# Kernel optimization log

Measured on AMD Instinct MI355X. Metric: run time of the kernel, lower is better.

Reference implementation:

```python
import jax, jax.numpy as jnp
import numpy as np

N, C, K, M, B = 100000, 128, 27, 60000, 8
CR = C // 4  # SE bottleneck
EPS = 1e-5

def sparse_conv(x, W, in_idx, out_idx, n_out):
    # gather-GEMM-scatter sparse conv: for each kernel offset k,
    # out[out_idx[k,m]] += W[k] @ x[in_idx[k,m]]
    g = x[in_idx]                                   # [K, M, Cin]
    y = jnp.einsum('kmc,kcd->kmd', g, W)            # [K, M, Cout]
    out = jnp.zeros((n_out, W.shape[-1]), x.dtype)
    return out.at[out_idx.reshape(-1)].add(y.reshape(-1, W.shape[-1]))

def batch_norm(x, gamma, beta):
    mu = jnp.mean(x, axis=0)
    var = jnp.var(x, axis=0)
    return (x - mu) * jax.lax.rsqrt(var + EPS) * gamma + beta

def setup_inputs() -> dict:
    key = jax.random.key(0)
    ks = jax.random.split(key, 10)
    x = jax.random.normal(ks[0], (N, C), dtype=jnp.float32)
    batch_id = jnp.sort(jax.random.randint(ks[1], (N,), 0, B))
    in_idx = jax.random.randint(ks[2], (K, M), 0, N)
    out_idx = jax.random.randint(ks[3], (K, M), 0, N)
    s = 1.0 / np.sqrt(C)
    W1 = jax.random.normal(ks[4], (K, C, C), dtype=jnp.float32) * s / np.sqrt(K)
    W2 = jax.random.normal(ks[5], (K, C, C), dtype=jnp.float32) * s / np.sqrt(K)
    fc1_w = jax.random.normal(ks[6], (C, CR), dtype=jnp.float32) * s
    fc2_w = jax.random.normal(ks[7], (CR, C), dtype=jnp.float32) / np.sqrt(CR)
    gamma1 = jnp.ones((C,), jnp.float32); beta1 = jnp.zeros((C,), jnp.float32)
    gamma2 = jnp.ones((C,), jnp.float32); beta2 = jnp.zeros((C,), jnp.float32)
    return {"x": x, "batch_id": batch_id, "in_idx": in_idx, "out_idx": out_idx,
            "W1": W1, "W2": W2, "fc1_w": fc1_w, "fc2_w": fc2_w,
            "gamma1": gamma1, "beta1": beta1, "gamma2": gamma2, "beta2": beta2}

def reference(x, batch_id, in_idx, out_idx, W1, W2, fc1_w, fc2_w,
              gamma1, beta1, gamma2, beta2):
    residual = x
    out = sparse_conv(x, W1, in_idx, out_idx, N)            # conv1
    out = jax.nn.relu(batch_norm(out, gamma1, beta1))       # norm1 + relu
    # SE squeeze: global sum pooling per batch
    pooled = jax.ops.segment_sum(out, batch_id, num_segments=B)  # [B, C]
    se = jax.nn.relu(pooled @ fc1_w)                        # fc1 + relu
    se = jax.nn.sigmoid(se @ fc2_w)                         # fc2 + sigmoid, [B, C]
    # per-segment gather-scale (replaces the Python loop over batches)
    out = out * se[batch_id]
    out = sparse_conv(out, W2, in_idx, out_idx, N)          # conv2
    out = batch_norm(out, gamma2, beta2)                    # norm2
    return jax.nn.relu(out + residual)
```

## Files before the change

### kernel.cpp

```cpp
#include <hip/hip_runtime.h>

#define NN 100000
#define CC 128
#define KK 27
#define MM 60000
#define NPAIR (KK * MM)
#define BBATCH 8
#define CRR 32
#define TM 64
#define NBLK ((MM + TM - 1) / TM)
#define NSB 98

typedef _Float16 half8 __attribute__((ext_vector_type(8)));
typedef float floatx4 __attribute__((ext_vector_type(4)));

struct __align__(8) Half4 { _Float16 x, y, z, w; };

__device__ __forceinline__ int cperm(int p) { return ((p & 7) << 4) | (p >> 3); }


__global__ __launch_bounds__(256) void convert_x_kernel(
    const float* __restrict__ x, _Float16* __restrict__ xh) {
    int i = blockIdx.x * 256 + threadIdx.x;
    if (i >= NN * (CC / 4)) return;
    float4 v = ((const float4*)x)[i];
    Half4 o;
    o.x = (_Float16)v.x; o.y = (_Float16)v.y;
    o.z = (_Float16)v.z; o.w = (_Float16)v.w;
    ((Half4*)xh)[i] = o;
}

__global__ __launch_bounds__(256) void transpose_w_kernel(
    const float* __restrict__ W, _Float16* __restrict__ Wt, int perm) {
    __shared__ float tile[32][33];
    int k = blockIdx.x >> 4;
    int tl = blockIdx.x & 15;
    int tr = (tl >> 2) * 32;
    int tc = (tl & 3) * 32;
    int c = threadIdx.x & 31;
    int r8 = threadIdx.x >> 5;
    const float* Wk = W + (size_t)k * CC * CC;
    _Float16* Wo = Wt + (size_t)k * CC * CC;
    #pragma unroll
    for (int i = 0; i < 4; ++i) {
        int r = r8 + i * 8;
        tile[r][c] = Wk[(tr + r) * CC + tc + c];
    }
    __syncthreads();
    #pragma unroll
    for (int i = 0; i < 4; ++i) {
        int r = r8 + i * 8;
        int ci = tr + c;
        int col = perm ? (((ci & 15) << 3) | (ci >> 4)) : ci;
        Wo[(tc + r) * CC + col] = (_Float16)tile[c][r];
    }
}


__global__ __launch_bounds__(256) void hist_kernel(
    const int* __restrict__ oidx, int* __restrict__ counts,
    int* __restrict__ seq, int GS) {
    int i = blockIdx.x * 256 + threadIdx.x;
    if (i < NPAIR) {
        int k = i / MM;
        int g = k / GS;
        seq[i] = atomicAdd(&counts[(size_t)g * NN + oidx[i]], 1);
    }
}

__global__ __launch_bounds__(256) void scan1_kernel(
    const int* __restrict__ counts, int* __restrict__ offsets, int* __restrict__ bsum) {
    __shared__ int ls[256];
    int g = blockIdx.y;
    const int* cg = counts + (size_t)g * NN;
    int* og = offsets + (size_t)g * (NN + 1);
    int b = blockIdx.x, t = threadIdx.x;
    int base = b * 1024 + t * 4;
    int v0 = (base + 0 < NN) ? cg[base + 0] : 0;
    int v1 = (base + 1 < NN) ? cg[base + 1] : 0;
    int v2 = (base + 2 < NN) ? cg[base + 2] : 0;
    int v3 = (base + 3 < NN) ? cg[base + 3] : 0;
    int s = v0 + v1 + v2 + v3;
    ls[t] = s;
    __syncthreads();
    for (int off = 1; off < 256; off <<= 1) {
        int x = (t >= off) ? ls[t - off] : 0;
        __syncthreads();
        if (t >= off) ls[t] += x;
        __syncthreads();
    }
    int ep = ls[t] - s;
    if (base + 0 < NN) og[base + 0] = ep;
    if (base + 1 < NN) og[base + 1] = ep + v0;
    if (base + 2 < NN) og[base + 2] = ep + v0 + v1;
    if (base + 3 < NN) og[base + 3] = ep + v0 + v1 + v2;
    if (t == 255) bsum[g * NSB + b] = ls[255];
}

__global__ void scan2_kernel(const int* __restrict__ bsum, int* __restrict__ bbase) {
    __shared__ int ls[128];
    int g = blockIdx.y;
    int t = threadIdx.x;
    int s = (t < NSB) ? bsum[g * NSB + t] : 0;
    ls[t] = s;
    __syncthreads();
    for (int off = 1; off < 128; off <<= 1) {
        int x = (t >= off) ? ls[t - off] : 0;
        __syncthreads();
        if (t >= off) ls[t] += x;
        __syncthreads();
    }
    if (t < NSB) bbase[g * NSB + t] = ls[t] - s;
}

__global__ __launch_bounds__(256) void scan3_kernel(
    int* __restrict__ offsets, const int* __restrict__ bbase, int GS) {
    int g = blockIdx.y;
    int* og = offsets + (size_t)g * (NN + 1);
    int b = blockIdx.x, t = threadIdx.x;
    int add = bbase[g * NSB + b];
    int base = b * 1024 + t * 4;
    #pragma unroll
    for (int i = 0; i < 4; ++i)
        if (base + i < NN) og[base + i] += add;
    if (b == 0 && t == 0) {
        int k0 = g * GS, k1 = min(KK, k0 + GS);
        og[NN] = (k1 - k0) * MM;
    }
}

__global__ __launch_bounds__(256) void ygemm_kernel(
    const _Float16* __restrict__ xh,
    const _Float16* __restrict__ Wt,
    const int* __restrict__ in_idx,
    const int* __restrict__ out_idx,
    const int* __restrict__ seq,
    const int* __restrict__ offG,
    _Float16* __restrict__ y,
    int k0)
{
    __shared__ __align__(16) _Float16 Blds[CC][136];
    int k  = k0 + blockIdx.x / NBLK;
    int tb = blockIdx.x % NBLK;
    int m0 = tb * TM;
    int tid = threadIdx.x;

    const _Float16* Wk = Wt + (size_t)k * CC * CC;
    #pragma unroll
    for (int i = 0; i < 8; ++i) {
        int ch = tid + i * 256;
        int r = ch >> 4;
        int c8 = (ch & 15) << 3;
        *(half8*)&Blds[r][c8] = *(const half8*)&Wk[r * CC + c8];
    }

    int w = tid >> 6, lane = tid & 63;
    int lr = lane & 15, lk = lane >> 4;

    int mr = m0 + w * 16 + lr;
    int mrc = min(mr, MM - 1);
    int g = in_idx[(size_t)k * MM + mrc];
    const _Float16* arow = &xh[(size_t)g * CC + lk * 8];
    half8 a0 = *(const half8*)(arow);
    half8 a1 = *(const half8*)(arow + 32);
    half8 a2 = *(const half8*)(arow + 64);
    half8 a3 = *(const half8*)(arow + 96);

    __syncthreads();

    floatx4 acc[8];
    #pragma unroll
    for (int f = 0; f < 8; ++f) acc[f] = (floatx4){0.f, 0.f, 0.f, 0.f};

    #pragma unroll
    for (int f = 0; f < 8; ++f)
        acc[f] = __builtin_amdgcn_mfma_f32_16x16x32_f16(a0, *(const half8*)&Blds[f * 16 + lr][0 * 32 + lk * 8], acc[f], 0, 0, 0);
    #pragma unroll
    for (int f = 0; f < 8; ++f)
        acc[f] = __builtin_amdgcn_mfma_f32_16x16x32_f16(a1, *(const half8*)&Blds[f * 16 + lr][1 * 32 + lk * 8], acc[f], 0, 0, 0);
    #pragma unroll
    for (int f = 0; f < 8; ++f)
        acc[f] = __builtin_amdgcn_mfma_f32_16x16x32_f16(a2, *(const half8*)&Blds[f * 16 + lr][2 * 32 + lk * 8], acc[f], 0, 0, 0);
    #pragma unroll
    for (int f = 0; f < 8; ++f)
        acc[f] = __builtin_amdgcn_mfma_f32_16x16x32_f16(a3, *(const half8*)&Blds[f * 16 + lr][3 * 32 + lk * 8], acc[f], 0, 0, 0);

    const int* oi = out_idx + (size_t)k * MM;
    const int* sq = seq + (size_t)k * MM;
    int rbase = w * 16 + lk * 4;
    #pragma unroll
    for (int j = 0; j < 4; ++j) {
        int m = m0 + rbase + j;
        if (m < MM) {
            int pos = offG[oi[m]] + sq[m];
            half8 hv;
            #pragma unroll
            for (int f = 0; f < 8; ++f) hv[f] = (_Float16)acc[f][j];
            *(half8*)&y[(size_t)pos * CC + lr * 8] = hv;
        }
    }
}

template<int MODE>
__global__ __launch_bounds__(256) void reduce_kernel(
    const _Float16* __restrict__ y, const int* __restrict__ offs,
    _Float16* __restrict__ outh) {
    int t = threadIdx.x;
    int o = blockIdx.x * 16 + (t >> 4);
    int l = t & 15;
    int s0 = offs[o], s1 = offs[o + 1];
    if (MODE == 1 && s0 == s1) return;
    float a[8] = {0.f, 0.f, 0.f, 0.f, 0.f, 0.f, 0.f, 0.f};
    for (int p = s0; p < s1; ++p) {
        half8 v = *(const half8*)&y[(size_t)p * CC + l * 8];
        #pragma unroll
        for (int i = 0; i < 8; ++i) a[i] += (float)v[i];
    }
    _Float16* op = outh + (size_t)o * CC + l * 8;
    if (MODE == 1) {
        half8 old = *(half8*)op;
        #pragma unroll
        for (int i = 0; i < 8; ++i) a[i] += (float)old[i];
    }
    half8 hv;
    #pragma unroll
    for (int i = 0; i < 8; ++i) hv[i] = (_Float16)a[i];
    *(half8*)op = hv;
}


__global__ __launch_bounds__(256) void bn_stats_f16_kernel(
    const _Float16* __restrict__ in, float* __restrict__ stats, int rpb) {
    int p = threadIdx.x & 127;
    int h = threadIdx.x >> 7;
    int r0 = blockIdx.x * rpb;
    int r1 = min(NN, r0 + rpb);
    float s = 0.f, s2 = 0.f;
    for (int r = r0 + h; r < r1; r += 2) {
        float v = (float)in[(size_t)r * CC + p];
        s += v; s2 += v * v;
    }
    __shared__ float ls[256], ls2[256];
    ls[threadIdx.x] = s; ls2[threadIdx.x] = s2;
    __syncthreads();
    if (h == 0) {
        atomicAdd(&stats[p],      ls[p] + ls[p + 128]);
        atomicAdd(&stats[CC + p], ls2[p] + ls2[p + 128]);
    }
}

__global__ __launch_bounds__(256) void bn_stats_f32_kernel(
    const float* __restrict__ in, float* __restrict__ stats, int rpb) {
    int p = threadIdx.x & 127;
    int h = threadIdx.x >> 7;
    int r0 = blockIdx.x * rpb;
    int r1 = min(NN, r0 + rpb);
    float s = 0.f, s2 = 0.f;
    for (int r = r0 + h; r < r1; r += 2) {
        float v = in[(size_t)r * CC + p];
        s += v; s2 += v * v;
    }
    __shared__ float ls[256], ls2[256];
    ls[threadIdx.x] = s; ls2[threadIdx.x] = s2;
    __syncthreads();
    if (h == 0) {
        atomicAdd(&stats[p],      ls[p] + ls[p + 128]);
        atomicAdd(&stats[CC + p], ls2[p] + ls2[p + 128]);
    }
}

__global__ void bn_finalize_kernel(
    const float* __restrict__ stats, const float* __restrict__ gamma,
    const float* __restrict__ beta, float* __restrict__ ss, int perm) {
    int p = threadIdx.x;
    if (p < CC) {
        int c = perm ? cperm(p) : p;
        float mean = stats[p] * (1.f / NN);
        float var = stats[CC + p] * (1.f / NN) - mean * mean;
        float sc = gamma[c] * rsqrtf(var + 1e-5f);
        ss[p] = sc;
        ss[CC + p] = beta[c] - mean * sc;
    }
}

__global__ __launch_bounds__(256) void pool_kernel(
    const _Float16* __restrict__ in, const float* __restrict__ ss,
    const int* __restrict__ batch_id, float* __restrict__ pooled, int rpb) {
    int p = threadIdx.x & 127;
    int h = threadIdx.x >> 7;
    float sc = ss[p], sh = ss[CC + p];
    int r0 = blockIdx.x * rpb;
    int r1 = min(NN, r0 + rpb);
    float acc = 0.f; int cur = -1;
    for (int r = r0 + h; r < r1; r += 2) {
        int b = batch_id[r];
        float v = fmaxf(fmaf((float)in[(size_t)r * CC + p], sc, sh), 0.f);
        if (b != cur) {
            if (cur >= 0) atomicAdd(&pooled[cur * CC + p], acc);
            cur = b; acc = 0.f;
        }
        acc += v;
    }
    if (cur >= 0) atomicAdd(&pooled[cur * CC + p], acc);
}

__global__ __launch_bounds__(256) void se_kernel(
    const float* __restrict__ pooled, const float* __restrict__ fc1,
    const float* __restrict__ fc2, float* __restrict__ se) {
    __shared__ float h[BBATCH][CRR];
    int tid = threadIdx.x;
    {
        int b = tid >> 5, j = tid & 31;
        float a = 0.f;
        for (int p = 0; p < CC; ++p) a += pooled[b * CC + p] * fc1[cperm(p) * CRR + j];
        h[b][j] = fmaxf(a, 0.f);
    }
    __syncthreads();
    #pragma unroll
    for (int i = 0; i < 4; ++i) {
        int idx = tid + i * 256;
        int b = idx >> 7, p = idx & 127;
        int c = cperm(p);
        float a = 0.f;
        #pragma unroll
        for (int j = 0; j < CRR; ++j) a += h[b][j] * fc2[j * CC + c];
        se[b * CC + p] = 1.f / (1.f + expf(-a));
    }
}

__global__ __launch_bounds__(256) void scale_convert_kernel(
    const _Float16* __restrict__ oh, const float* __restrict__ ss,
    const float* __restrict__ se, const int* __restrict__ batch_id,
    _Float16* __restrict__ xo) {
    int idx = blockIdx.x * 256 + threadIdx.x;
    if (idx >= NN * 16) return;
    int row = idx >> 4;
    int l = idx & 15;
    int b = batch_id[row];
    half8 v = *(const half8*)(oh + (size_t)row * CC + l * 8);
    half8 o;
    #pragma unroll
    for (int i = 0; i < 8; ++i) {
        int p = l * 8 + i;
        float t = fmaxf(fmaf((float)v[i], ss[p], ss[CC + p]), 0.f) * se[b * CC + p];
        o[i] = (_Float16)t;
    }
    *(half8*)(xo + (size_t)row * CC + l * 8) = o;
}

__global__ __launch_bounds__(256) void final2_kernel(
    const _Float16* __restrict__ oh, const float* __restrict__ ss,
    const float* __restrict__ x, float* __restrict__ dout) {
    int idx = blockIdx.x * 256 + threadIdx.x;
    if (idx >= NN * 16) return;
    int row = idx >> 4;
    int l = idx & 15;
    half8 v = *(const half8*)(oh + (size_t)row * CC + l * 8);
    #pragma unroll
    for (int i = 0; i < 8; ++i) {
        int p = l * 8 + i;
        int c = (i << 4) | l;
        float r = x[(size_t)row * CC + c];
        dout[(size_t)row * CC + c] = fmaxf(fmaf((float)v[i], ss[p], ss[CC + p]) + r, 0.f);
    }
}

__global__ __launch_bounds__(256) void conv_kernel(
    const _Float16* __restrict__ xh, const _Float16* __restrict__ Wt,
    const int* __restrict__ in_idx, const int* __restrict__ out_idx,
    float* __restrict__ out) {
    __shared__ __align__(16) _Float16 Alds[TM][136];
    __shared__ __align__(16) _Float16 Blds[CC][136];
    int k  = blockIdx.x / NBLK;
    int tb = blockIdx.x % NBLK;
    int m0 = tb * TM;
    int tid = threadIdx.x;
    const _Float16* Wk = Wt + (size_t)k * CC * CC;
    #pragma unroll
    for (int i = 0; i < 8; ++i) {
        int ch = tid + i * 256;
        int r = ch >> 4, c8 = (ch & 15) << 3;
        *(half8*)&Blds[r][c8] = *(const half8*)&Wk[r * CC + c8];
    }
    const int* ii = in_idx + (size_t)k * MM + m0;
    #pragma unroll
    for (int i = 0; i < 4; ++i) {
        int r = (tid >> 4) + i * 16, c8 = (tid & 15) << 3;
        if (m0 + r < MM) {
            int g = ii[r];
            *(half8*)&Alds[r][c8] = *(const half8*)&xh[(size_t)g * CC + c8];
        } else { half8 z = {}; *(half8*)&Alds[r][c8] = z; }
    }
    __syncthreads();
    int w = tid >> 6, lane = tid & 63;
    int lr = lane & 15, lk = lane >> 4;
    floatx4 acc[8];
    #pragma unroll
    for (int f = 0; f < 8; ++f) acc[f] = (floatx4){0.f, 0.f, 0.f, 0.f};
    #pragma unroll
    for (int kc = 0; kc < 4; ++kc) {
        half8 a = *(const half8*)&Alds[w * 16 + lr][kc * 32 + lk * 8];
        #pragma unroll
        for (int f = 0; f < 8; ++f) {
            half8 bb = *(const half8*)&Blds[f * 16 + lr][kc * 32 + lk * 8];
            acc[f] = __builtin_amdgcn_mfma_f32_16x16x32_f16(a, bb, acc[f], 0, 0, 0);
        }
    }
    const int* oi = out_idx + (size_t)k * MM + m0;
    int mb = w * 16 + lk * 4;
    #pragma unroll
    for (int j = 0; j < 4; ++j) {
        int m = m0 + mb + j;
        if (m < MM) {
            int o = oi[mb + j];
            float* orow = out + (size_t)o * CC + lr;
            #pragma unroll
            for (int f = 0; f < 8; ++f)
                atomicAdd(orow + f * 16, acc[f][j]);
        }
    }
}

__global__ __launch_bounds__(256) void c2p_kernel(
    const float* __restrict__ in, _Float16* __restrict__ outh) {
    int i = blockIdx.x * 256 + threadIdx.x;
    if (i >= NN * CC) return;
    int row = i >> 7, p = i & 127;
    outh[i] = (_Float16)in[(size_t)row * CC + cperm(p)];
}

__global__ __launch_bounds__(256) void final_kernel(
    float* __restrict__ out, const float* __restrict__ ss,
    const float* __restrict__ x) {
    int i = blockIdx.x * 256 + threadIdx.x;
    if (i >= NN * (CC / 4)) return;
    int q = i & 31;
    float4 v  = ((float4*)out)[i];
    float4 r  = ((const float4*)x)[i];
    float4 sc = ((const float4*)ss)[q];
    float4 sh = ((const float4*)(ss + CC))[q];
    float4 o;
    o.x = fmaxf(fmaf(v.x, sc.x, sh.x) + r.x, 0.f);
    o.y = fmaxf(fmaf(v.y, sc.y, sh.y) + r.y, 0.f);
    o.z = fmaxf(fmaf(v.z, sc.z, sh.z) + r.z, 0.f);
    o.w = fmaxf(fmaf(v.w, sc.w, sh.w) + r.w, 0.f);
    ((float4*)out)[i] = o;
}

extern "C" void kernel_launch(void* const* d_in, const int* in_sizes, int n_in,
                              void* d_out, int out_size, void* d_ws, size_t ws_size,
                              hipStream_t stream) {
    const float* x        = (const float*)d_in[0];
    const int*   batch_id = (const int*)d_in[1];
    const int*   in_idx   = (const int*)d_in[2];
    const int*   out_idx  = (const int*)d_in[3];
    const float* W1       = (const float*)d_in[4];
    const float* W2       = (const float*)d_in[5];
    const float* fc1      = (const float*)d_in[6];
    const float* fc2      = (const float*)d_in[7];
    const float* gamma1   = (const float*)d_in[8];
    const float* beta1    = (const float*)d_in[9];
    const float* gamma2   = (const float*)d_in[10];
    const float* beta2    = (const float*)d_in[11];
    float* out = (float*)d_out;

    char* ws = (char*)d_ws;
    auto al = [](size_t v) { return (v + 255) & ~(size_t)255; };

    size_t o_xh = 0;
    size_t o_w1 = al(o_xh + (size_t)NN * CC * 2);
    size_t o_w2 = al(o_w1 + (size_t)KK * CC * CC * 2);
    size_t o_oh = al(o_w2 + (size_t)KK * CC * CC * 2);
    size_t o_sm = al(o_oh + (size_t)NN * CC * 2);
    size_t fixed_end = al(o_sm + 6 * 4096);

    static const int PL[10] = {3, 4, 5, 6, 7, 9, 14, 27, 2, 1};
    int P = -1, GS = 0;
    size_t o_cnt = 0, o_off = 0, o_bs = 0, o_bb = 0, o_seq = 0, o_y = 0;
    for (int t = 0; t < 10; ++t) {
        int p = PL[t];
        int gs = (KK + p - 1) / p;
        size_t a = fixed_end;
        size_t c0 = a; a = al(a + (size_t)p * NN * 4);
        size_t c1 = a; a = al(a + (size_t)p * (NN + 1) * 4);
        size_t c2 = a; a = al(a + (size_t)p * NSB * 4);
        size_t c3 = a; a = al(a + (size_t)p * NSB * 4);
        size_t c4 = a; a = al(a + (size_t)NPAIR * 4);
        size_t c5 = a; a = al(a + (size_t)gs * MM * CC * 2);
        if (a <= ws_size) {
            P = p; GS = gs;
            o_cnt = c0; o_off = c1; o_bs = c2; o_bb = c3; o_seq = c4; o_y = c5;
            break;
        }
    }

    _Float16* xh  = (_Float16*)(ws + o_xh);
    _Float16* w1t = (_Float16*)(ws + o_w1);
    _Float16* w2t = (_Float16*)(ws + o_w2);
    _Float16* oh  = (_Float16*)(ws + o_oh);
    float* stats1 = (float*)(ws + o_sm);
    float* ss1    = stats1 + 256;
    float* stats2 = ss1 + 256;
    float* ss2    = stats2 + 256;
    float* pooled = ss2 + 256;
    float* sebuf  = pooled + BBATCH * CC;

    int g_e4 = (NN * (CC / 4) + 255) / 256;
    int g_16 = (NN * 16 + 255) / 256;
    int g_pair = (NPAIR + 255) / 256;
    int rpb = (NN + 2047) / 2048;

    convert_x_kernel<<<g_e4, 256, 0, stream>>>(x, xh);
    transpose_w_kernel<<<KK * 16, 256, 0, stream>>>(W1, w1t, 0);
    transpose_w_kernel<<<KK * 16, 256, 0, stream>>>(W2, w2t, 1);

    hipMemsetAsync(stats1, 0, 2 * CC * 4, stream);
    hipMemsetAsync(stats2, 0, 2 * CC * 4, stream);
    hipMemsetAsync(pooled, 0, BBATCH * CC * 4, stream);

    if (P > 0) {
        int* counts  = (int*)(ws + o_cnt);
        int* offsets = (int*)(ws + o_off);
        int* bsum    = (int*)(ws + o_bs);
        int* bbase   = (int*)(ws + o_bb);
        int* seq     = (int*)(ws + o_seq);
        _Float16* ybuf = (_Float16*)(ws + o_y);

        hipMemsetAsync(counts, 0, (size_t)P * NN * 4, stream);
        hist_kernel<<<g_pair, 256, 0, stream>>>(out_idx, counts, seq, GS);
        scan1_kernel<<<dim3(NSB, P), 256, 0, stream>>>(counts, offsets, bsum);
        scan2_kernel<<<dim3(1, P), 128, 0, stream>>>(bsum, bbase);
        scan3_kernel<<<dim3(NSB, P), 256, 0, stream>>>(offsets, bbase, GS);

        for (int g = 0; g < P; ++g) {
            int k0 = g * GS, k1 = min(KK, k0 + GS), kn = k1 - k0;
            if (kn <= 0) break;
            const int* offG = offsets + (size_t)g * (NN + 1);
            ygemm_kernel<<<kn * NBLK, 256, 0, stream>>>(xh, w1t, in_idx, out_idx, seq, offG, ybuf, k0);
            if (g == 0) reduce_kernel<0><<<NN / 16, 256, 0, stream>>>(ybuf, offG, oh);
            else        reduce_kernel<1><<<NN / 16, 256, 0, stream>>>(ybuf, offG, oh);
        }

        bn_stats_f16_kernel<<<2048, 256, 0, stream>>>(oh, stats1, rpb);
        bn_finalize_kernel<<<1, 128, 0, stream>>>(stats1, gamma1, beta1, ss1, 1);
        pool_kernel<<<2048, 256, 0, stream>>>(oh, ss1, batch_id, pooled, rpb);
        se_kernel<<<1, 256, 0, stream>>>(pooled, fc1, fc2, sebuf);
        scale_convert_kernel<<<g_16, 256, 0, stream>>>(oh, ss1, sebuf, batch_id, xh);

        for (int g = 0; g < P; ++g) {
            int k0 = g * GS, k1 = min(KK, k0 + GS), kn = k1 - k0;
            if (kn <= 0) break;
            const int* offG = offsets + (size_t)g * (NN + 1);
            ygemm_kernel<<<kn * NBLK, 256, 0, stream>>>(xh, w2t, in_idx, out_idx, seq, offG, ybuf, k0);
            if (g == 0) reduce_kernel<0><<<NN / 16, 256, 0, stream>>>(ybuf, offG, oh);
            else        reduce_kernel<1><<<NN / 16, 256, 0, stream>>>(ybuf, offG, oh);
        }

        bn_stats_f16_kernel<<<2048, 256, 0, stream>>>(oh, stats2, rpb);
        bn_finalize_kernel<<<1, 128, 0, stream>>>(stats2, gamma2, beta2, ss2, 1);
        final2_kernel<<<g_16, 256, 0, stream>>>(oh, ss2, x, out);
    } else {
        hipMemsetAsync(out, 0, (size_t)NN * CC * 4, stream);
        conv_kernel<<<KK * NBLK, 256, 0, stream>>>(xh, w1t, in_idx, out_idx, out);
        c2p_kernel<<<(NN * CC + 255) / 256, 256, 0, stream>>>(out, oh);

        bn_stats_f16_kernel<<<2048, 256, 0, stream>>>(oh, stats1, rpb);
        bn_finalize_kernel<<<1, 128, 0, stream>>>(stats1, gamma1, beta1, ss1, 1);
        pool_kernel<<<2048, 256, 0, stream>>>(oh, ss1, batch_id, pooled, rpb);
        se_kernel<<<1, 256, 0, stream>>>(pooled, fc1, fc2, sebuf);
        scale_convert_kernel<<<g_16, 256, 0, stream>>>(oh, ss1, sebuf, batch_id, xh);

        hipMemsetAsync(out, 0, (size_t)NN * CC * 4, stream);
        conv_kernel<<<KK * NBLK, 256, 0, stream>>>(xh, w2t, in_idx, out_idx, out);

        bn_stats_f32_kernel<<<2048, 256, 0, stream>>>(out, stats2, rpb);
        bn_finalize_kernel<<<1, 128, 0, stream>>>(stats2, gamma2, beta2, ss2, 0);
        final_kernel<<<g_e4, 256, 0, stream>>>(out, ss2, x);
    }
}
```

Baseline: 889.3 us.

## Double-buffer y slices and overlap gather-GEMM with previous slice reduction

Merges the histogram, x conversion and both weight transposes into one prolog launch. Conv is restructured so each launch runs the GEMM for slice g and the segmented reduction for slice g-1 in the same grid, using two y buffers so the two stages overlap. BN statistics are fused into the last reduction pass, which removes a separate full pass over the conv output. Double buffering uses more workspace, so fewer kernel groups may fit, and the shared-memory stats reduction adds atomics.

New measurement: 1.136 ms. +27.7%, slower.

```diff
diff --git a/kernel.cpp b/kernel.cpp
--- a/kernel.cpp
+++ b/kernel.cpp
@@ -10,6 +10,10 @@
 #define TM 64
 #define NBLK ((MM + TM - 1) / TM)
 #define NSB 98
+#define GPAIR_BLKS ((NPAIR + 255) / 256)
+#define GE4_BLKS (NN * (CC / 4) / 256)
+#define TRB (KK * 16)
+#define GRED (NN / 16)
 
 typedef _Float16 half8 __attribute__((ext_vector_type(8)));
 typedef float floatx4 __attribute__((ext_vector_type(4)));
@@ -18,55 +22,56 @@
 
 __device__ __forceinline__ int cperm(int p) { return ((p & 7) << 4) | (p >> 3); }
 
-
-__global__ __launch_bounds__(256) void convert_x_kernel(
-    const float* __restrict__ x, _Float16* __restrict__ xh) {
-    int i = blockIdx.x * 256 + threadIdx.x;
-    if (i >= NN * (CC / 4)) return;
-    float4 v = ((const float4*)x)[i];
-    Half4 o;
-    o.x = (_Float16)v.x; o.y = (_Float16)v.y;
-    o.z = (_Float16)v.z; o.w = (_Float16)v.w;
-    ((Half4*)xh)[i] = o;
-}
-
-__global__ __launch_bounds__(256) void transpose_w_kernel(
-    const float* __restrict__ W, _Float16* __restrict__ Wt, int perm) {
+__global__ __launch_bounds__(256) void prolog_kernel(
+    const int* __restrict__ oidx, int* __restrict__ counts, int* __restrict__ seq, int GS,
+    const float* __restrict__ x, _Float16* __restrict__ xh,
+    const float* __restrict__ W1, _Float16* __restrict__ w1t,
+    const float* __restrict__ W2, _Float16* __restrict__ w2t)
+{
     __shared__ float tile[32][33];
-    int k = blockIdx.x >> 4;
-    int tl = blockIdx.x & 15;
-    int tr = (tl >> 2) * 32;
-    int tc = (tl & 3) * 32;
-    int c = threadIdx.x & 31;
-    int r8 = threadIdx.x >> 5;
-    const float* Wk = W + (size_t)k * CC * CC;
-    _Float16* Wo = Wt + (size_t)k * CC * CC;
-    #pragma unroll
-    for (int i = 0; i < 4; ++i) {
-        int r = r8 + i * 8;
-        tile[r][c] = Wk[(tr + r) * CC + tc + c];
-    }
-    __syncthreads();
-    #pragma unroll
-    for (int i = 0; i < 4; ++i) {
-        int r = r8 + i * 8;
-        int ci = tr + c;
-        int col = perm ? (((ci & 15) << 3) | (ci >> 4)) : ci;
-        Wo[(tc + r) * CC + col] = (_Float16)tile[c][r];
-    }
-}
-
-
-__global__ __launch_bounds__(256) void hist_kernel(
-    const int* __restrict__ oidx, int* __restrict__ counts,
-    int* __restrict__ seq, int GS) {
-    int i = blockIdx.x * 256 + threadIdx.x;
-    if (i < NPAIR) {
-        int k = i / MM;
-        int g = k / GS;
-        seq[i] = atomicAdd(&counts[(size_t)g * NN + oidx[i]], 1);
-    }
-}
+    int b = blockIdx.x;
+    if (b < GPAIR_BLKS) {
+        int i = b * 256 + threadIdx.x;
+        if (i < NPAIR) {
+            int g = (i / MM) / GS;
+            seq[i] = atomicAdd(&counts[(size_t)g * NN + oidx[i]], 1);
+        }
+    } else if (b < GPAIR_BLKS + GE4_BLKS) {
+        int i = (b - GPAIR_BLKS) * 256 + threadIdx.x;
+        float4 v = ((const float4*)x)[i];
+        Half4 o;
+        o.x = (_Float16)v.x; o.y = (_Float16)v.y;
+        o.z = (_Float16)v.z; o.w = (_Float16)v.w;
+        ((Half4*)xh)[i] = o;
+    } else {
+        int tb = b - GPAIR_BLKS - GE4_BLKS;
+        const float* W; _Float16* Wo; int perm;
+        if (tb < TRB) { W = W1; Wo = w1t; perm = 0; }
+        else          { tb -= TRB; W = W2; Wo = w2t; perm = 1; }
+        int k = tb >> 4;
+        int tl = tb & 15;
+        int tr = (tl >> 2) * 32;
+        int tc = (tl & 3) * 32;
+        int c = threadIdx.x & 31;
+        int r8 = threadIdx.x >> 5;
+        const float* Wk = W + (size_t)k * CC * CC;
+        _Float16* WoK = Wo + (size_t)k * CC * CC;
+        #pragma unroll
+        for (int i = 0; i < 4; ++i) {
+            int r = r8 + i * 8;
+            tile[r][c] = Wk[(tr + r) * CC + tc + c];
+        }
+        __syncthreads();
+        #pragma unroll
+        for (int i = 0; i < 4; ++i) {
+            int r = r8 + i * 8;
+            int ci = tr + c;
+            int col = perm ? (((ci & 15) << 3) | (ci >> 4)) : ci;
+            WoK[(tc + r) * CC + col] = (_Float16)tile[c][r];
+        }
+    }
+}
+
 
 __global__ __launch_bounds__(256) void scan1_kernel(
     const int* __restrict__ counts, int* __restrict__ offsets, int* __restrict__ bsum) {
@@ -129,145 +134,132 @@
     }
 }
 
-__global__ __launch_bounds__(256) void ygemm_kernel(
-    const _Float16* __restrict__ xh,
-    const _Float16* __restrict__ Wt,
-    const int* __restrict__ in_idx,
-    const int* __restrict__ out_idx,
+__global__ __launch_bounds__(256) void pipe_kernel(
+    const _Float16* __restrict__ xh, const _Float16* __restrict__ Wt,
+    const int* __restrict__ in_idx, const int* __restrict__ out_idx,
     const int* __restrict__ seq,
-    const int* __restrict__ offG,
-    _Float16* __restrict__ y,
-    int k0)
+    const int* __restrict__ offY, _Float16* __restrict__ yY, int k0, int kn,
+    const int* __restrict__ offR, const _Float16* __restrict__ yR,
+    _Float16* __restrict__ oh, float* __restrict__ stats, int mode)
 {
     __shared__ __align__(16) _Float16 Blds[CC][136];
-    int k  = k0 + blockIdx.x / NBLK;
-    int tb = blockIdx.x % NBLK;
-    int m0 = tb * TM;
-    int tid = threadIdx.x;
-
-    const _Float16* Wk = Wt + (size_t)k * CC * CC;
-    #pragma unroll
-    for (int i = 0; i < 8; ++i) {
-        int ch = tid + i * 256;
-        int r = ch >> 4;
-        int c8 = (ch & 15) << 3;
-        *(half8*)&Blds[r][c8] = *(const half8*)&Wk[r * CC + c8];
-    }
-
-    int w = tid >> 6, lane = tid & 63;
-    int lr = lane & 15, lk = lane >> 4;
-
-    int mr = m0 + w * 16 + lr;
-    int mrc = min(mr, MM - 1);
-    int g = in_idx[(size_t)k * MM + mrc];
-    const _Float16* arow = &xh[(size_t)g * CC + lk * 8];
-    half8 a0 = *(const half8*)(arow);
-    half8 a1 = *(const half8*)(arow + 32);
-    half8 a2 = *(const half8*)(arow + 64);
-    half8 a3 = *(const half8*)(arow + 96);
-
-    __syncthreads();
-
-    floatx4 acc[8];
-    #pragma unroll
-    for (int f = 0; f < 8; ++f) acc[f] = (floatx4){0.f, 0.f, 0.f, 0.f};
-
-    #pragma unroll
-    for (int f = 0; f < 8; ++f)
-        acc[f] = __builtin_amdgcn_mfma_f32_16x16x32_f16(a0, *(const half8*)&Blds[f * 16 + lr][0 * 32 + lk * 8], acc[f], 0, 0, 0);
-    #pragma unroll
-    for (int f = 0; f < 8; ++f)
-        acc[f] = __builtin_amdgcn_mfma_f32_16x16x32_f16(a1, *(const half8*)&Blds[f * 16 + lr][1 * 32 + lk * 8], acc[f], 0, 0, 0);
-    #pragma unroll
-    for (int f = 0; f < 8; ++f)
-        acc[f] = __builtin_amdgcn_mfma_f32_16x16x32_f16(a2, *(const half8*)&Blds[f * 16 + lr][2 * 32 + lk * 8], acc[f], 0, 0, 0);
-    #pragma unroll
-    for (int f = 0; f < 8; ++f)
-        acc[f] = __builtin_amdgcn_mfma_f32_16x16x32_f16(a3, *(const half8*)&Blds[f * 16 + lr][3 * 32 + lk * 8], acc[f], 0, 0, 0);
-
-    const int* oi = out_idx + (size_t)k * MM;
-    const int* sq = seq + (size_t)k * MM;
-    int rbase = w * 16 + lk * 4;
-    #pragma unroll
-    for (int j = 0; j < 4; ++j) {
-        int m = m0 + rbase + j;
-        if (m < MM) {
-            int pos = offG[oi[m]] + sq[m];
+    __shared__ float lsum[CC], lsq[CC];
+    int nyb = kn * NBLK;
+    if ((int)blockIdx.x < nyb) {
+        int k  = k0 + blockIdx.x / NBLK;
+        int tb = blockIdx.x % NBLK;
+        int m0 = tb * TM;
+        int tid = threadIdx.x;
+
+        const _Float16* Wk = Wt + (size_t)k * CC * CC;
+        #pragma unroll
+        for (int i = 0; i < 8; ++i) {
+            int ch = tid + i * 256;
+            int r = ch >> 4;
+            int c8 = (ch & 15) << 3;
+            *(half8*)&Blds[r][c8] = *(const half8*)&Wk[r * CC + c8];
+        }
+
+        int w = tid >> 6, lane = tid & 63;
+        int lr = lane & 15, lk = lane >> 4;
+
+        int mr = m0 + w * 16 + lr;
+        int mrc = min(mr, MM - 1);
+        int g = in_idx[(size_t)k * MM + mrc];
+        const _Float16* arow = &xh[(size_t)g * CC + lk * 8];
+        half8 a0 = *(const half8*)(arow);
+        half8 a1 = *(const half8*)(arow + 32);
+        half8 a2 = *(const half8*)(arow + 64);
+        half8 a3 = *(const half8*)(arow + 96);
+
+        __syncthreads();
+
+        floatx4 acc[8];
+        #pragma unroll
+        for (int f = 0; f < 8; ++f) acc[f] = (floatx4){0.f, 0.f, 0.f, 0.f};
+        #pragma unroll
+        for (int f = 0; f < 8; ++f)
+            acc[f] = __builtin_amdgcn_mfma_f32_16x16x32_f16(a0, *(const half8*)&Blds[f * 16 + lr][0 * 32 + lk * 8], acc[f], 0, 0, 0);
+        #pragma unroll
+        for (int f = 0; f < 8; ++f)
+            acc[f] = __builtin_amdgcn_mfma_f32_16x16x32_f16(a1, *(const half8*)&Blds[f * 16 + lr][1 * 32 + lk * 8], acc[f], 0, 0, 0);
+        #pragma unroll
+        for (int f = 0; f < 8; ++f)
+            acc[f] = __builtin_amdgcn_mfma_f32_16x16x32_f16(a2, *(const half8*)&Blds[f * 16 + lr][2 * 32 + lk * 8], acc[f], 0, 0, 0);
+        #pragma unroll
+        for (int f = 0; f < 8; ++f)
+            acc[f] = __builtin_amdgcn_mfma_f32_16x16x32_f16(a3, *(const half8*)&Blds[f * 16 + lr][3 * 32 + lk * 8], acc[f], 0, 0, 0);
+
+        const int* oi = out_idx + (size_t)k * MM;
+        const int* sq = seq + (size_t)k * MM;
+        int rbase = w * 16 + lk * 4;
+        #pragma unroll
+        for (int j = 0; j < 4; ++j) {
+            int m = m0 + rbase + j;
+            if (m < MM) {
+                int pos = offY[oi[m]] + sq[m];
+                half8 hv;
+                #pragma unroll
+                for (int f = 0; f < 8; ++f) hv[f] = (_Float16)acc[f][j];
+                *(half8*)&yY[(size_t)pos * CC + lr * 8] = hv;
+            }
+        }
+    } else {
+        if (mode < 0) return;
+        int blk = blockIdx.x - nyb;
+        int t = threadIdx.x;
+        int o = blk * 16 + (t >> 4);
+        int l = t & 15;
+        int s0 = offR[o], s1 = offR[o + 1];
+        bool active = !(mode == 1 && s0 == s1);
+        float a[8] = {0.f, 0.f, 0.f, 0.f, 0.f, 0.f, 0.f, 0.f};
+        if (active) {
+            for (int p = s0; p < s1; ++p) {
+                half8 v = *(const half8*)&yR[(size_t)p * CC + l * 8];
+                #pragma unroll
+                for (int i = 0; i < 8; ++i) a[i] += (float)v[i];
+            }
+            _Float16* op = oh + (size_t)o * CC + l * 8;
+            if (mode >= 1) {
+                half8 old = *(half8*)op;
+                #pragma unroll
+                for (int i = 0; i < 8; ++i) a[i] += (float)old[i];
+            }
             half8 hv;
             #pragma unroll
-            for (int f = 0; f < 8; ++f) hv[f] = (_Float16)acc[f][j];
-            *(half8*)&y[(size_t)pos * CC + lr * 8] = hv;
-        }
-    }
-}
-
-template<int MODE>
-__global__ __launch_bounds__(256) void reduce_kernel(
-    const _Float16* __restrict__ y, const int* __restrict__ offs,
-    _Float16* __restrict__ outh) {
-    int t = threadIdx.x;
-    int o = blockIdx.x * 16 + (t >> 4);
-    int l = t & 15;
-    int s0 = offs[o], s1 = offs[o + 1];
-    if (MODE == 1 && s0 == s1) return;
-    float a[8] = {0.f, 0.f, 0.f, 0.f, 0.f, 0.f, 0.f, 0.f};
-    for (int p = s0; p < s1; ++p) {
-        half8 v = *(const half8*)&y[(size_t)p * CC + l * 8];
-        #pragma unroll
-        for (int i = 0; i < 8; ++i) a[i] += (float)v[i];
-    }
-    _Float16* op = outh + (size_t)o * CC + l * 8;
-    if (MODE == 1) {
-        half8 old = *(half8*)op;
-        #pragma unroll
-        for (int i = 0; i < 8; ++i) a[i] += (float)old[i];
-    }
-    half8 hv;
-    #pragma unroll
-    for (int i = 0; i < 8; ++i) hv[i] = (_Float16)a[i];
-    *(half8*)op = hv;
-}
-
-
-__global__ __launch_bounds__(256) void bn_stats_f16_kernel(
-    const _Float16* __restrict__ in, float* __restrict__ stats, int rpb) {
-    int p = threadIdx.x & 127;
-    int h = threadIdx.x >> 7;
-    int r0 = blockIdx.x * rpb;
-    int r1 = min(NN, r0 + rpb);
-    float s = 0.f, s2 = 0.f;
-    for (int r = r0 + h; r < r1; r += 2) {
-        float v = (float)in[(size_t)r * CC + p];
-        s += v; s2 += v * v;
-    }
-    __shared__ float ls[256], ls2[256];
-    ls[threadIdx.x] = s; ls2[threadIdx.x] = s2;
-    __syncthreads();
-    if (h == 0) {
-        atomicAdd(&stats[p],      ls[p] + ls[p + 128]);
-        atomicAdd(&stats[CC + p], ls2[p] + ls2[p + 128]);
-    }
-}
-
-__global__ __launch_bounds__(256) void bn_stats_f32_kernel(
-    const float* __restrict__ in, float* __restrict__ stats, int rpb) {
-    int p = threadIdx.x & 127;
-    int h = threadIdx.x >> 7;
-    int r0 = blockIdx.x * rpb;
-    int r1 = min(NN, r0 + rpb);
-    float s = 0.f, s2 = 0.f;
-    for (int r = r0 + h; r < r1; r += 2) {
-        float v = in[(size_t)r * CC + p];
-        s += v; s2 += v * v;
-    }
-    __shared__ float ls[256], ls2[256];
-    ls[threadIdx.x] = s; ls2[threadIdx.x] = s2;
-    __syncthreads();
-    if (h == 0) {
-        atomicAdd(&stats[p],      ls[p] + ls[p + 128]);
-        atomicAdd(&stats[CC + p], ls2[p] + ls2[p + 128]);
-    }
-}
+            for (int i = 0; i < 8; ++i) hv[i] = (_Float16)a[i];
+            *(half8*)op = hv;
+        }
+        if (mode == 2) {
+            float sq_[8];
+            #pragma unroll
+            for (int i = 0; i < 8; ++i) sq_[i] = a[i] * a[i];
+            #pragma unroll
+            for (int off = 16; off < 64; off <<= 1) {
+                #pragma unroll
+                for (int i = 0; i < 8; ++i) {
+                    a[i]   += __shfl_xor(a[i], off);
+                    sq_[i] += __shfl_xor(sq_[i], off);
+                }
+            }
+            if (t < CC) { lsum[t] = 0.f; lsq[t] = 0.f; }
+            __syncthreads();
+            if ((t & 63) < 16) {
+                #pragma unroll
+                for (int i = 0; i < 8; ++i) {
+                    atomicAdd(&lsum[l * 8 + i], a[i]);
+                    atomicAdd(&lsq[l * 8 + i], sq_[i]);
+                }
+            }
+            __syncthreads();
+            if (t < CC) {
+                atomicAdd(&stats[t], lsum[t]);
+                atomicAdd(&stats[CC + t], lsq[t]);
+            }
+        }
+    }
+}
+
 
 __global__ void bn_finalize_kernel(
     const float* __restrict__ stats, const float* __restrict__ gamma,
@@ -365,6 +357,43 @@
     }
 }
 
+__global__ __launch_bounds__(256) void convert_x_kernel(
+    const float* __restrict__ x, _Float16* __restrict__ xh) {
+    int i = blockIdx.x * 256 + threadIdx.x;
+    if (i >= NN * (CC / 4)) return;
+    float4 v = ((const float4*)x)[i];
+    Half4 o;
+    o.x = (_Float16)v.x; o.y = (_Float16)v.y;
+    o.z = (_Float16)v.z; o.w = (_Float16)v.w;
+    ((Half4*)xh)[i] = o;
+}
+
+__global__ __launch_bounds__(256) void transpose_w_kernel(
+    const float* __restrict__ W, _Float16* __restrict__ Wt, int perm) {
+    __shared__ float tile[32][33];
+    int k = blockIdx.x >> 4;
+    int tl = blockIdx.x & 15;
+    int tr = (tl >> 2) * 32;
+    int tc = (tl & 3) * 32;
+    int c = threadIdx.x & 31;
+    int r8 = threadIdx.x >> 5;
+    const float* Wk = W + (size_t)k * CC * CC;
+    _Float16* Wo = Wt + (size_t)k * CC * CC;
+    #pragma unroll
+    for (int i = 0; i < 4; ++i) {
+        int r = r8 + i * 8;
+        tile[r][c] = Wk[(tr + r) * CC + tc + c];
+    }
+    __syncthreads();
+    #pragma unroll
+    for (int i = 0; i < 4; ++i) {
+        int r = r8 + i * 8;
+        int ci = tr + c;
+        int col = perm ? (((ci & 15) << 3) | (ci >> 4)) : ci;
+        Wo[(tc + r) * CC + col] = (_Float16)tile[c][r];
+    }
+}
+
 __global__ __launch_bounds__(256) void conv_kernel(
     const _Float16* __restrict__ xh, const _Float16* __restrict__ Wt,
     const int* __restrict__ in_idx, const int* __restrict__ out_idx,
@@ -418,6 +447,46 @@
             for (int f = 0; f < 8; ++f)
                 atomicAdd(orow + f * 16, acc[f][j]);
         }
+    }
+}
+
+__global__ __launch_bounds__(256) void bn_stats_f16_kernel(
+    const _Float16* __restrict__ in, float* __restrict__ stats, int rpb) {
+    int p = threadIdx.x & 127;
+    int h = threadIdx.x >> 7;
+    int r0 = blockIdx.x * rpb;
+    int r1 = min(NN, r0 + rpb);
+    float s = 0.f, s2 = 0.f;
+    for (int r = r0 + h; r < r1; r += 2) {
+        float v = (float)in[(size_t)r * CC + p];
+        s += v; s2 += v * v;
+    }
+    __shared__ float ls[256], ls2[256];
+    ls[threadIdx.x] = s; ls2[threadIdx.x] = s2;
+    __syncthreads();
+    if (h == 0) {
+        atomicAdd(&stats[p],      ls[p] + ls[p + 128]);
+        atomicAdd(&stats[CC + p], ls2[p] + ls2[p + 128]);
+    }
+}
+
+__global__ __launch_bounds__(256) void bn_stats_f32_kernel(
+    const float* __restrict__ in, float* __restrict__ stats, int rpb) {
+    int p = threadIdx.x & 127;
+    int h = threadIdx.x >> 7;
+    int r0 = blockIdx.x * rpb;
+    int r1 = min(NN, r0 + rpb);
+    float s = 0.f, s2 = 0.f;
+    for (int r = r0 + h; r < r1; r += 2) {
+        float v = in[(size_t)r * CC + p];
+        s += v; s2 += v * v;
+    }
+    __shared__ float ls[256], ls2[256];
+    ls[threadIdx.x] = s; ls2[threadIdx.x] = s2;
+    __syncthreads();
+    if (h == 0) {
+        atomicAdd(&stats[p],      ls[p] + ls[p + 128]);
+        atomicAdd(&stats[CC + p], ls2[p] + ls2[p + 128]);
     }
 }
 
@@ -474,23 +543,31 @@
     size_t o_sm = al(o_oh + (size_t)NN * CC * 2);
     size_t fixed_end = al(o_sm + 6 * 4096);
 
-    static const int PL[10] = {3, 4, 5, 6, 7, 9, 14, 27, 2, 1};
-    int P = -1, GS = 0;
+    static const int PL2[7] = {4, 5, 6, 7, 9, 14, 27};
+    static const int PL1[9] = {3, 4, 5, 6, 7, 9, 14, 27, 2};
+    int P = -1, GS = 0, NSL = 0;
     size_t o_cnt = 0, o_off = 0, o_bs = 0, o_bb = 0, o_seq = 0, o_y = 0;
-    for (int t = 0; t < 10; ++t) {
-        int p = PL[t];
-        int gs = (KK + p - 1) / p;
-        size_t a = fixed_end;
-        size_t c0 = a; a = al(a + (size_t)p * NN * 4);
-        size_t c1 = a; a = al(a + (size_t)p * (NN + 1) * 4);
-        size_t c2 = a; a = al(a + (size_t)p * NSB * 4);
-        size_t c3 = a; a = al(a + (size_t)p * NSB * 4);
-        size_t c4 = a; a = al(a + (size_t)NPAIR * 4);
-        size_t c5 = a; a = al(a + (size_t)gs * MM * CC * 2);
-        if (a <= ws_size) {
-            P = p; GS = gs;
-            o_cnt = c0; o_off = c1; o_bs = c2; o_bb = c3; o_seq = c4; o_y = c5;
-            break;
+    size_t slice_elems = 0;
+    for (int pass = 0; pass < 2 && P < 0; ++pass) {
+        int nsl = (pass == 0) ? 2 : 1;
+        const int* L = (pass == 0) ? PL2 : PL1;
+        int nL = (pass == 0) ? 7 : 9;
+        for (int t = 0; t < nL; ++t) {
+            int p = L[t];
+            int gs = (KK + p - 1) / p;
+            size_t a = fixed_end;
+            size_t c0 = a; a = al(a + (size_t)p * NN * 4);
+            size_t c1 = a; a = al(a + (size_t)p * (NN + 1) * 4);
+            size_t c2 = a; a = al(a + (size_t)p * NSB * 4);
+            size_t c3 = a; a = al(a + (size_t)p * NSB * 4);
+            size_t c4 = a; a = al(a + (size_t)NPAIR * 4);
+            size_t c5 = a; a = al(a + (size_t)nsl * gs * MM * CC * 2);
+            if (a <= ws_size) {
+                P = p; GS = gs; NSL = nsl;
+                o_cnt = c0; o_off = c1; o_bs = c2; o_bb = c3; o_seq = c4; o_y = c5;
+                slice_elems = (size_t)gs * MM * CC;
+                break;
+            }
         }
     }
 
@@ -505,41 +582,85 @@
     float* pooled = ss2 + 256;
     float* sebuf  = pooled + BBATCH * CC;
 
-    int g_e4 = (NN * (CC / 4) + 255) / 256;
     int g_16 = (NN * 16 + 255) / 256;
-    int g_pair = (NPAIR + 255) / 256;
     int rpb = (NN + 2047) / 2048;
-
-    convert_x_kernel<<<g_e4, 256, 0, stream>>>(x, xh);
-    transpose_w_kernel<<<KK * 16, 256, 0, stream>>>(W1, w1t, 0);
-    transpose_w_kernel<<<KK * 16, 256, 0, stream>>>(W2, w2t, 1);
 
     hipMemsetAsync(stats1, 0, 2 * CC * 4, stream);
     hipMemsetAsync(stats2, 0, 2 * CC * 4, stream);
     hipMemsetAsync(pooled, 0, BBATCH * CC * 4, stream);
 
     if (P > 0) {
-        int* counts  = (int*)(ws + o_cnt);
-        int* offsets = (int*)(ws + o_off);
-        int* bsum    = (int*)(ws + o_bs);
-        int* bbase   = (int*)(ws + o_bb);
-        int* seq     = (int*)(ws + o_seq);
-        _Float16* ybuf = (_Float16*)(ws + o_y);
+        int* counts   = (int*)(ws + o_cnt);
+        int* offsets  = (int*)(ws + o_off);
+        int* bsum     = (int*)(ws + o_bs);
+        int* bbase    = (int*)(ws + o_bb);
+        int* seq      = (int*)(ws + o_seq);
+        _Float16* yb0 = (_Float16*)(ws + o_y);
+        _Float16* yb1 = yb0 + ((NSL == 2) ? slice_elems : 0);
 
         hipMemsetAsync(counts, 0, (size_t)P * NN * 4, stream);
-        hist_kernel<<<g_pair, 256, 0, stream>>>(out_idx, counts, seq, GS);
+        prolog_kernel<<<GPAIR_BLKS + GE4_BLKS + 2 * TRB, 256, 0, stream>>>(
+            out_idx, counts, seq, GS, x, xh, W1, w1t, W2, w2t);
         scan1_kernel<<<dim3(NSB, P), 256, 0, stream>>>(counts, offsets, bsum);
         scan2_kernel<<<dim3(1, P), 128, 0, stream>>>(bsum, bbase);
         scan3_kernel<<<dim3(NSB, P), 256, 0, stream>>>(offsets, bbase, GS);
 
-        for (int g = 0; g < P; ++g) {
-            int k0 = g * GS, k1 = min(KK, k0 + GS), kn = k1 - k0;
-            if (kn <= 0) break;
-            const int* offG = offsets + (size_t)g * (NN + 1);
-            ygemm_kernel<<<kn * NBLK, 256, 0, stream>>>(xh, w1t, in_idx, out_idx, seq, offG, ybuf, k0);
-            if (g == 0) reduce_kernel<0><<<NN / 16, 256, 0, stream>>>(ybuf, offG, oh);
-            else        reduce_kernel<1><<<NN / 16, 256, 0, stream>>>(ybuf, offG, oh);
-        }
+        auto run_conv = [&](const _Float16* Wt, float* stats) {
+            if (NSL == 2) {
+                for (int g = 0; g < P; ++g) {
+                    int k0 = g * GS, kn = min(KK, k0 + GS) - k0;
+                    _Float16* yg = (g & 1) ? yb1 : yb0;
+                    const int* offY = offsets + (size_t)g * (NN + 1);
+                    if (g == 0) {
+                        pipe_kernel<<<kn * NBLK, 256, 0, stream>>>(
+                            xh, Wt, in_idx, out_idx, seq,
+                            offY, yg, k0, kn, offY, yg, oh, stats, -1);
+                    } else {
+                        const int* offR = offsets + (size_t)(g - 1) * (NN + 1);
+                        const _Float16* yR = ((g - 1) & 1) ? yb1 : yb0;
+                        pipe_kernel<<<kn * NBLK + GRED, 256, 0, stream>>>(
+                            xh, Wt, in_idx, out_idx, seq,
+                            offY, yg, k0, kn, offR, yR, oh, stats, (g == 1) ? 0 : 1);
+                    }
+                }
+                const int* offL = offsets + (size_t)(P - 1) * (NN + 1);
+                const _Float16* yL = ((P - 1) & 1) ? yb1 : yb0;
+                pipe_kernel<<<GRED, 256, 0, stream>>>(
+                    xh, Wt, in_idx, out_idx, seq,
+                    offL, yb0, 0, 0, offL, yL, oh, stats, 2);
+            } else {
+                for (int g = 0; g < P; ++g) {
+                    int k0 = g * GS, kn = min(KK, k0 + GS) - k0;
+                    const int* offg = offsets + (size_t)g * (NN + 1);
+                    pipe_kernel<<<kn * NBLK, 256, 0, stream>>>(
+                        xh, Wt, in_idx, out_idx, seq,
+                        offg, yb0, k0, kn, offg, yb0, oh, stats, -1);
+                    int mode = (g == 0) ? 0 : ((g == P - 1) ? 2 : 1);
+                    pipe_kernel<<<GRED, 256, 0, stream>>>(
+                        xh, Wt, in_idx, out_idx, seq,
+                        offg, yb0, 0, 0, offg, yb0, oh, stats, mode);
+                }
+            }
+        };
+
+        run_conv(w1t, stats1);
+        bn_finalize_kernel<<<1, 128, 0, stream>>>(stats1, gamma1, beta1, ss1, 1);
+        pool_kernel<<<2048, 256, 0, stream>>>(oh, ss1, batch_id, pooled, rpb);
+        se_kernel<<<1, 256, 0, stream>>>(pooled, fc1, fc2, sebuf);
+        scale_convert_kernel<<<g_16, 256, 0, stream>>>(oh, ss1, sebuf, batch_id, xh);
+
+        run_conv(w2t, stats2);
+        bn_finalize_kernel<<<1, 128, 0, stream>>>(stats2, gamma2, beta2, ss2, 1);
+        final2_kernel<<<g_16, 256, 0, stream>>>(oh, ss2, x, out);
+    } else {
+        int g_e4 = GE4_BLKS;
+        convert_x_kernel<<<g_e4, 256, 0, stream>>>(x, xh);
+        transpose_w_kernel<<<TRB, 256, 0, stream>>>(W1, w1t, 0);
+        transpose_w_kernel<<<TRB, 256, 0, stream>>>(W2, w2t, 1);
+
+        hipMemsetAsync(out, 0, (size_t)NN * CC * 4, stream);
+        conv_kernel<<<KK * NBLK, 256, 0, stream>>>(xh, w1t, in_idx, out_idx, out);
+        c2p_kernel<<<(NN * CC + 255) / 256, 256, 0, stream>>>(out, oh);
 
         bn_stats_f16_kernel<<<2048, 256, 0, stream>>>(oh, stats1, rpb);
         bn_finalize_kernel<<<1, 128, 0, stream>>>(stats1, gamma1, beta1, ss1, 1);
@@ -547,29 +668,6 @@
         se_kernel<<<1, 256, 0, stream>>>(pooled, fc1, fc2, sebuf);
         scale_convert_kernel<<<g_16, 256, 0, stream>>>(oh, ss1, sebuf, batch_id, xh);
 
-        for (int g = 0; g < P; ++g) {
-            int k0 = g * GS, k1 = min(KK, k0 + GS), kn = k1 - k0;
-            if (kn <= 0) break;
-            const int* offG = offsets + (size_t)g * (NN + 1);
-            ygemm_kernel<<<kn * NBLK, 256, 0, stream>>>(xh, w2t, in_idx, out_idx, seq, offG, ybuf, k0);
-            if (g == 0) reduce_kernel<0><<<NN / 16, 256, 0, stream>>>(ybuf, offG, oh);
-            else        reduce_kernel<1><<<NN / 16, 256, 0, stream>>>(ybuf, offG, oh);
-        }
-
-        bn_stats_f16_kernel<<<2048, 256, 0, stream>>>(oh, stats2, rpb);
-        bn_finalize_kernel<<<1, 128, 0, stream>>>(stats2, gamma2, beta2, ss2, 1);
-        final2_kernel<<<g_16, 256, 0, stream>>>(oh, ss2, x, out);
-    } else {
-        hipMemsetAsync(out, 0, (size_t)NN * CC * 4, stream);
-        conv_kernel<<<KK * NBLK, 256, 0, stream>>>(xh, w1t, in_idx, out_idx, out);
-        c2p_kernel<<<(NN * CC + 255) / 256, 256, 0, stream>>>(out, oh);
-
-        bn_stats_f16_kernel<<<2048, 256, 0, stream>>>(oh, stats1, rpb);
-        bn_finalize_kernel<<<1, 128, 0, stream>>>(stats1, gamma1, beta1, ss1, 1);
-        pool_kernel<<<2048, 256, 0, stream>>>(oh, ss1, batch_id, pooled, rpb);
-        se_kernel<<<1, 256, 0, stream>>>(pooled, fc1, fc2, sebuf);
-        scale_convert_kernel<<<g_16, 256, 0, stream>>>(oh, ss1, sebuf, batch_id, xh);
-
         hipMemsetAsync(out, 0, (size_t)NN * CC * 4, stream);
         conv_kernel<<<KK * NBLK, 256, 0, stream>>>(xh, w2t, in_idx, out_idx, out);
 
```
